# Optimization experiments

Hardware: AMD Instinct MI355X
Metric: run time of the kernel (lower is better)

## Reference

```python
import jax, jax.numpy as jnp
import numpy as np
from jax import lax


def setup_inputs() -> dict:
    key = jax.random.key(0)
    k1, k2 = jax.random.split(key)
    L, B, D = 1024, 16, 1024
    x = jax.random.normal(k1, (L, B, D), dtype=jnp.float32)
    # weight maps n_in -> n_out*k with k=3 (n_in == n_out); small scale for stability
    weight = jax.random.normal(k2, (D, 3 * D), dtype=jnp.float32) * 0.05
    bias = jnp.zeros((2 * D,), dtype=jnp.float32)
    c0 = jnp.zeros((B, D), dtype=jnp.float32)
    return {"x": x, "weight": weight, "bias": bias, "c0": c0}


def reference(x, weight, bias, c0):
    # SRUCell forward, k == 3 (n_in == n_out), unidirectional, tanh activation,
    # no dropout masks (mask_h == NULL -> mask = 1).
    L, B, D = x.shape
    u = (x.reshape(L * B, D) @ weight).reshape(L, B, D, 3)
    b1 = bias[:D]
    b2 = bias[D:]
    u0 = u[..., 0]                                   # [L, B, D]
    g1 = jax.nn.sigmoid(u[..., 1] + b1)              # forget gate
    g2 = jax.nn.sigmoid(u[..., 2] + b2)              # reset/highway gate

    def step(c, inp):
        u0_t, g1_t, g2_t, x_t = inp
        c_new = (c - u0_t) * g1_t + u0_t             # c = c'*g1 + u0*(1-g1)
        h_t = (jnp.tanh(c_new) - x_t) * g2_t + x_t   # h = act(c)*g2 + x*(1-g2)
        return c_new, h_t

    c_last, h = lax.scan(step, c0, (u0, g1, g2, x))
    return h, c_last
```

## Files before the change

kernel.cpp:

```cpp
#include <hip/hip_runtime.h>

#define L_DIM 1024
#define B_DIM 16
#define D_DIM 1024
#define K_DIM 1024
#define N_DIM 3072
#define M_DIM (L_DIM * B_DIM)
#define CHAINS 16384

typedef float f32x4 __attribute__((ext_vector_type(4)));
typedef __bf16 bf16x8 __attribute__((ext_vector_type(8)));
typedef unsigned short u16;
typedef unsigned int u32;

__device__ __forceinline__ u16 f2bf(float f) {
  u32 u = __float_as_uint(f);
  u = u + 0x7FFFu + ((u >> 16) & 1u);
  return (u16)(u >> 16);
}
__device__ __forceinline__ float bf2f(u16 v) {
  return __uint_as_float(((u32)v) << 16);
}
__device__ __forceinline__ float bf2f_lo(u32 v) {
  return __uint_as_float(v << 16);
}
__device__ __forceinline__ float bf2f_hi(u32 v) {
  return __uint_as_float(v & 0xffff0000u);
}
__device__ __forceinline__ float fexp(float v) {
  return __builtin_amdgcn_exp2f(v * 1.4426950408889634f);
}
__device__ __forceinline__ float sigm(float z) {
  return __builtin_amdgcn_rcpf(1.0f + fexp(-z));
}
__device__ __forceinline__ float ftanh(float v) {
  return 1.0f - 2.0f * __builtin_amdgcn_rcpf(1.0f + fexp(2.0f * v));
}

__global__ __launch_bounds__(256) void cvt_fused(const float4* __restrict__ xin,
                                                 ushort4* __restrict__ xout,
                                                 const float* __restrict__ W,
                                                 u16* __restrict__ Wt) {
  if (blockIdx.x < 16384) {
    int i = blockIdx.x * 256 + threadIdx.x;
    float4 v = xin[i];
    ushort4 o;
    o.x = f2bf(v.x); o.y = f2bf(v.y); o.z = f2bf(v.z); o.w = f2bf(v.w);
    xout[i] = o;
  } else {
    __shared__ float tile[64][65];
    int wb = blockIdx.x - 16384;
    int c0 = (wb % 48) * 64;
    int r0 = (wb / 48) * 64;
    int tx = threadIdx.x & 63;
    int ty = threadIdx.x >> 6;
#pragma unroll
    for (int i = 0; i < 16; ++i) {
      int row = i * 4 + ty;
      tile[row][tx] = W[(size_t)(r0 + row) * N_DIM + c0 + tx];
    }
    __syncthreads();
#pragma unroll
    for (int i = 0; i < 16; ++i) {
      int crow = i * 4 + ty;
      int c = c0 + crow;
      int nprime = (c % 3) * D_DIM + (c / 3);
      Wt[(size_t)nprime * K_DIM + r0 + tx] = f2bf(tile[tx][crow]);
    }
  }
}


#define AS1 __attribute__((address_space(1)))
#define AS3 __attribute__((address_space(3)))
#define STAGE(gp, lp) do { \
  __builtin_amdgcn_global_load_lds((const AS1 void*)(gp), (AS3 void*)(lp), 16, 0, 0); \
  __builtin_amdgcn_global_load_lds((const AS1 void*)((gp) + (size_t)64 * K_DIM), \
                                   (AS3 void*)((lp) + 4096), 16, 0, 0); \
} while (0)

#define QUAD(AI, JB, BF) \
  _Pragma("unroll") \
  for (int i = 0; i < 4; ++i) { \
    _Pragma("unroll") \
    for (int j = 0; j < 2; ++j) { \
      acc[AI + i][JB + j] = __builtin_amdgcn_mfma_f32_16x16x32_bf16(aF[i][0], BF[j][0], acc[AI + i][JB + j], 0, 0, 0); \
      acc[AI + i][JB + j] = __builtin_amdgcn_mfma_f32_16x16x32_bf16(aF[i][1], BF[j][1], acc[AI + i][JB + j], 0, 0, 0); \
    } \
  }

__global__ __launch_bounds__(512, 2) void gemm_kernel(const u16* __restrict__ A,
                                                      const u16* __restrict__ Bt,
                                                      u16* __restrict__ U) {
  __shared__ __align__(16) u16 sm[81920];
  const int tid = threadIdx.x;
  const int wave = tid >> 6;
  const int lane = tid & 63;
  const int wm = wave >> 2;
  const int wn = wave & 3;
  const int quad = lane >> 4;
  const int l16 = lane & 15;

  const int flat = blockIdx.y * 12 + blockIdx.x;
  const int swz = (flat & 7) * 96 + (flat >> 3);
  const int m0 = (swz / 12) * 256;
  const int n0 = (swz % 12) * 256;

  const int rr = tid >> 3;
  const int slot = (tid & 7) ^ (rr & 7);
  const u16* gA = A + (size_t)(m0 + rr) * K_DIM + slot * 8;
  const u16* gB = Bt + (size_t)(n0 + rr) * K_DIM + slot * 8;

  u16* ldsA = sm + wave * 512;
  u16* ldsB = sm + 32768 + wave * 512;

  const int swzu = (l16 & 7) << 3;
  const int c0 = (quad * 8) ^ swzu;
  const int c1 = (32 + quad * 8) ^ swzu;
  const u16* pA = sm + (wm * 128 + l16) * 64;
  const u16* pB = sm + 32768 + (wn * 64 + l16) * 64;

  f32x4 acc[8][4] = {};

  STAGE(gA, ldsA);
  STAGE(gA + (size_t)128 * K_DIM, ldsA + 8192);
  STAGE(gB, ldsB);
  STAGE(gB + (size_t)128 * K_DIM, ldsB + 8192);
  STAGE(gB + 64, ldsB + 16384);
  STAGE(gB + (size_t)128 * K_DIM + 64, ldsB + 16384 + 8192);
  asm volatile("s_waitcnt vmcnt(4)" ::: "memory");
  __builtin_amdgcn_s_barrier();

  int su = 0;
  int st = 2;
  for (int u = 0; u < 16; ++u) {
    const int abuf = u & 1;
    const int anb = abuf ^ 1;
    const u16* pAb = pA + abuf * 16384;
    const u16* pBb = pB + su * 16384;
    bf16x8 aF[4][2], bLo[2][2], bHi[2][2];

#pragma unroll
    for (int i = 0; i < 4; ++i) {
      aF[i][0] = *(const bf16x8*)(pAb + i * 1024 + c0);
      aF[i][1] = *(const bf16x8*)(pAb + i * 1024 + c1);
    }
#pragma unroll
    for (int j = 0; j < 2; ++j) {
      bLo[j][0] = *(const bf16x8*)(pBb + j * 1024 + c0);
      bLo[j][1] = *(const bf16x8*)(pBb + j * 1024 + c1);
      bHi[j][0] = *(const bf16x8*)(pBb + (2 + j) * 1024 + c0);
      bHi[j][1] = *(const bf16x8*)(pBb + (2 + j) * 1024 + c1);
    }
    if (u < 15) {
      STAGE(gA + (u + 1) * 64, ldsA + anb * 16384);
      STAGE(gA + (size_t)128 * K_DIM + (u + 1) * 64, ldsA + anb * 16384 + 8192);
    }
    __builtin_amdgcn_s_setprio(1);
    QUAD(0, 0, bLo)
    QUAD(0, 2, bHi)
    __builtin_amdgcn_s_setprio(0);

#pragma unroll
    for (int i = 0; i < 4; ++i) {
      aF[i][0] = *(const bf16x8*)(pAb + (4 + i) * 1024 + c0);
      aF[i][1] = *(const bf16x8*)(pAb + (4 + i) * 1024 + c1);
    }
    if (u < 14) {
      STAGE(gB + (u + 2) * 64, ldsB + st * 16384);
      STAGE(gB + (size_t)128 * K_DIM + (u + 2) * 64, ldsB + st * 16384 + 8192);
    }
    __builtin_amdgcn_s_setprio(1);
    QUAD(4, 2, bHi)
    QUAD(4, 0, bLo)
    __builtin_amdgcn_s_setprio(0);

    if (u < 14) {
      asm volatile("s_waitcnt vmcnt(4)" ::: "memory");
    } else if (u == 14) {
      asm volatile("s_waitcnt vmcnt(0)" ::: "memory");
    }
    __builtin_amdgcn_s_barrier();

    su = (su == 2) ? 0 : su + 1;
    st = (st == 2) ? 0 : st + 1;
  }

#pragma unroll
  for (int i = 0; i < 8; ++i) {
#pragma unroll
    for (int j = 0; j < 4; ++j) {
      const int col = n0 + wn * 64 + j * 16 + l16;
      const int rb = m0 + wm * 128 + i * 16 + quad * 4;
#pragma unroll
      for (int r = 0; r < 4; ++r)
        U[(size_t)(rb + r) * N_DIM + col] = f2bf(acc[i][j][r]);
    }
  }
}

__global__ __launch_bounds__(512) void sru_onepass(const u16* __restrict__ U,
                                                   const float* __restrict__ x,
                                                   const float* __restrict__ bias,
                                                   const float* __restrict__ c0,
                                                   float* __restrict__ h,
                                                   float* __restrict__ clast) {
  __shared__ float sU0[2][32][33];
  __shared__ float sG1[2][32][33];
  __shared__ float sG2[2][32][33];
  __shared__ float sCC[2][32][33];

  const int flat = blockIdx.x;
  const int cb = (flat & 7) * 64 + (flat >> 3);
  const int b  = cb >> 5;
  const int d0 = (cb & 31) << 5;
  const int t  = threadIdx.x;
  const int s  = t >> 4;
  const int ch = (t & 15) * 2;
  const int d2 = d0 + ch;

  const float2 bb1 = *(const float2*)(bias + d2);
  const float2 bb2 = *(const float2*)(bias + D_DIM + d2);

  float creg = 0.0f;
  if (t < 32) creg = c0[cb * 32 + t];

  u32 w0, w1, w2;
  float2 xv;
  {
    const size_t m = (size_t)(s * 16 + b);
    const u16* p = U + m * N_DIM + d2;
    w0 = *(const u32*)p;
    w1 = *(const u32*)(p + D_DIM);
    w2 = *(const u32*)(p + 2 * D_DIM);
    xv = *(const float2*)(x + m * D_DIM + d2);
  }

  for (int k = 0; k <= 32; ++k) {
    const int cur = k & 1;
    const int prv = cur ^ 1;

    float2 xcons = xv;

    if (k < 32) {
      sU0[cur][ch][s]     = bf2f_lo(w0);
      sU0[cur][ch + 1][s] = bf2f_hi(w0);
      sG1[cur][ch][s]     = sigm(bf2f_lo(w1) + bb1.x);
      sG1[cur][ch + 1][s] = sigm(bf2f_hi(w1) + bb1.y);
      sG2[cur][ch][s]     = sigm(bf2f_lo(w2) + bb2.x);
      sG2[cur][ch + 1][s] = sigm(bf2f_hi(w2) + bb2.y);
      if (k < 31) {
        const size_t m = (size_t)(((k + 1) * 32 + s) * 16 + b);
        const u16* p = U + m * N_DIM + d2;
        w0 = *(const u32*)p;
        w1 = *(const u32*)(p + D_DIM);
        w2 = *(const u32*)(p + 2 * D_DIM);
      }
      xv = *(const float2*)(x + (size_t)((k * 32 + s) * 16 + b) * D_DIM + d2);
    }
    if (k >= 1) {
      const size_t m = (size_t)(((k - 1) * 32 + s) * 16 + b);
      float ca  = sCC[prv][ch][s];
      float cbv = sCC[prv][ch + 1][s];
      float ga  = sG2[prv][ch][s];
      float gb  = sG2[prv][ch + 1][s];
      float2 hv;
      hv.x = (ftanh(ca) - xcons.x) * ga + xcons.x;
      hv.y = (ftanh(cbv) - xcons.y) * gb + xcons.y;
      *(float2*)(h + m * D_DIM + d2) = hv;
    }
    asm volatile("s_waitcnt lgkmcnt(0)" ::: "memory");
    __builtin_amdgcn_s_barrier();

    if (k < 32 && t < 32) {
      float lu[16], lg[16];
#pragma unroll
      for (int q = 0; q < 16; ++q) { lu[q] = sU0[cur][t][q]; lg[q] = sG1[cur][t][q]; }
#pragma unroll
      for (int q = 0; q < 16; ++q) {
        creg = (creg - lu[q]) * lg[q] + lu[q];
        sCC[cur][t][q] = creg;
      }
#pragma unroll
      for (int q = 0; q < 16; ++q) { lu[q] = sU0[cur][t][16 + q]; lg[q] = sG1[cur][t][16 + q]; }
#pragma unroll
      for (int q = 0; q < 16; ++q) {
        creg = (creg - lu[q]) * lg[q] + lu[q];
        sCC[cur][t][16 + q] = creg;
      }
    }
    asm volatile("s_waitcnt lgkmcnt(0)" ::: "memory");
    __builtin_amdgcn_s_barrier();
  }

  if (t < 32) clast[cb * 32 + t] = creg;
}

extern "C" void kernel_launch(void* const* d_in, const int* in_sizes, int n_in,
                              void* d_out, int out_size, void* d_ws, size_t ws_size,
                              hipStream_t stream) {
  const float* x = (const float*)d_in[0];
  const float* W = (const float*)d_in[1];
  const float* bias = (const float*)d_in[2];
  const float* c0 = (const float*)d_in[3];
  float* out = (float*)d_out;

  char* ws = (char*)d_ws;
  u16* xb = (u16*)ws;
  u16* wt = (u16*)(ws + 33554432);
  u16* U = (u16*)(ws + 33554432 + 6291456);

  cvt_fused<<<16384 + 768, 256, 0, stream>>>((const float4*)x, (ushort4*)xb, W, wt);
  gemm_kernel<<<dim3(N_DIM / 256, M_DIM / 256), 512, 0, stream>>>(xb, wt, U);
  sru_onepass<<<512, 512, 0, stream>>>(U, x, bias, c0, out, out + (size_t)M_DIM * D_DIM);
}
```

Measured before the change: 260.7 us.

## Move h output computation to non-scan waves to overlap with serial scan

The h output (tanh, gate blend, store) for the previous chunk now runs on waves 1-7 (threads 64+) in the same phase as wave 0's serial recurrence scan, instead of before the barrier on all threads. The first 64 threads are freed so the scan wave is not delayed by output work, and seven waves cover the 512 elements with some handling two. This aims to hide output and x-load latency behind the sequential scan, at the cost of uneven per-thread work and extra index arithmetic.

Result: faster. 255.2 us (-2.1%).

```diff
diff --git a/kernel.cpp b/kernel.cpp
--- a/kernel.cpp
+++ b/kernel.cpp
@@ -199,6 +199,7 @@
   }
 }
 
+
 __global__ __launch_bounds__(512) void sru_onepass(const u16* __restrict__ U,
                                                    const float* __restrict__ x,
                                                    const float* __restrict__ bias,
@@ -222,25 +223,31 @@
   const float2 bb1 = *(const float2*)(bias + d2);
   const float2 bb2 = *(const float2*)(bias + D_DIM + d2);
 
+  const int i1 = t - 64;
+  const int s1 = i1 >> 4, ch1 = (i1 & 15) * 2;
+  const int i2 = 448 + (t - 64);
+  const int s2 = i2 >> 4, ch2 = (i2 & 15) * 2;
+
   float creg = 0.0f;
   if (t < 32) creg = c0[cb * 32 + t];
 
   u32 w0, w1, w2;
-  float2 xv;
+  float2 xv1, xv2;
   {
     const size_t m = (size_t)(s * 16 + b);
     const u16* p = U + m * N_DIM + d2;
     w0 = *(const u32*)p;
     w1 = *(const u32*)(p + D_DIM);
     w2 = *(const u32*)(p + 2 * D_DIM);
-    xv = *(const float2*)(x + m * D_DIM + d2);
-  }
+  }
+  if (t >= 64)             xv1 = *(const float2*)(x + (size_t)(s1 * 16 + b) * D_DIM + d0 + ch1);
+  if (t >= 64 && t < 128)  xv2 = *(const float2*)(x + (size_t)(s2 * 16 + b) * D_DIM + d0 + ch2);
 
   for (int k = 0; k <= 32; ++k) {
     const int cur = k & 1;
     const int prv = cur ^ 1;
 
-    float2 xcons = xv;
+    float2 xc1 = xv1, xc2 = xv2;
 
     if (k < 32) {
       sU0[cur][ch][s]     = bf2f_lo(w0);
@@ -256,18 +263,8 @@
         w1 = *(const u32*)(p + D_DIM);
         w2 = *(const u32*)(p + 2 * D_DIM);
       }
-      xv = *(const float2*)(x + (size_t)((k * 32 + s) * 16 + b) * D_DIM + d2);
-    }
-    if (k >= 1) {
-      const size_t m = (size_t)(((k - 1) * 32 + s) * 16 + b);
-      float ca  = sCC[prv][ch][s];
-      float cbv = sCC[prv][ch + 1][s];
-      float ga  = sG2[prv][ch][s];
-      float gb  = sG2[prv][ch + 1][s];
-      float2 hv;
-      hv.x = (ftanh(ca) - xcons.x) * ga + xcons.x;
-      hv.y = (ftanh(cbv) - xcons.y) * gb + xcons.y;
-      *(float2*)(h + m * D_DIM + d2) = hv;
+      if (t >= 64)            xv1 = *(const float2*)(x + (size_t)((k * 32 + s1) * 16 + b) * D_DIM + d0 + ch1);
+      if (t >= 64 && t < 128) xv2 = *(const float2*)(x + (size_t)((k * 32 + s2) * 16 + b) * D_DIM + d0 + ch2);
     }
     asm volatile("s_waitcnt lgkmcnt(0)" ::: "memory");
     __builtin_amdgcn_s_barrier();
@@ -289,11 +286,35 @@
         sCC[cur][t][16 + q] = creg;
       }
     }
+    if (k >= 1 && t >= 64) {
+      {
+        const size_t m = (size_t)(((k - 1) * 32 + s1) * 16 + b);
+        float ca  = sCC[prv][ch1][s1];
+        float cbv = sCC[prv][ch1 + 1][s1];
+        float ga  = sG2[prv][ch1][s1];
+        float gb  = sG2[prv][ch1 + 1][s1];
+        float2 hv;
+        hv.x = (ftanh(ca) - xc1.x) * ga + xc1.x;
+        hv.y = (ftanh(cbv) - xc1.y) * gb + xc1.y;
+        *(float2*)(h + m * D_DIM + d0 + ch1) = hv;
+      }
+      if (t < 128) {
+        const size_t m = (size_t)(((k - 1) * 32 + s2) * 16 + b);
+        float ca  = sCC[prv][ch2][s2];
+        float cbv = sCC[prv][ch2 + 1][s2];
+        float ga  = sG2[prv][ch2][s2];
+        float gb  = sG2[prv][ch2 + 1][s2];
+        float2 hv;
+        hv.x = (ftanh(ca) - xc2.x) * ga + xc2.x;
+        hv.y = (ftanh(cbv) - xc2.y) * gb + xc2.y;
+        *(float2*)(h + m * D_DIM + d0 + ch2) = hv;
+      }
+    }
     asm volatile("s_waitcnt lgkmcnt(0)" ::: "memory");
     __builtin_amdgcn_s_barrier();
-  }
-
-  if (t < 32) clast[cb * 32 + t] = creg;
+
+    if (k == 32 && t < 32) clast[cb * 32 + t] = creg;
+  }
 }
 
 extern "C" void kernel_launch(void* const* d_in, const int* in_sizes, int n_in,
```
